# Optimization experiments

Hardware: AMD Instinct MI355X
Metric: run time of the kernel (lower is better)

## Reference

```python
import jax, jax.numpy as jnp
import numpy as np

N = 50000   # num_nodes
E = 640000  # num_edges (avg degree ~12.8)
D = 128     # input_dim
H = 128     # hidden_dim
T = 100     # targets per head


def setup_inputs() -> dict:
    key = jax.random.key(0)
    ks = jax.random.split(key, 20)
    w = lambda k, s: jax.random.normal(k, s, jnp.float32) * 0.02
    return {
        "x": jax.random.normal(ks[0], (N, D), jnp.float32),
        "edge_index": jax.random.randint(ks[1], (2, E), 0, N, dtype=jnp.int32),
        "edge_weight": jax.random.uniform(ks[2], (E,), jnp.float32),
        "ace_idx": jax.random.randint(ks[3], (T,), 0, N, dtype=jnp.int32),
        "h2_idx": jax.random.randint(ks[4], (T,), 0, N, dtype=jnp.int32),
        "W1": w(ks[5], (D, H)), "b1": jnp.zeros((H,), jnp.float32),
        "W2": w(ks[6], (H, H)), "b2": jnp.zeros((H,), jnp.float32),
        "W3": w(ks[7], (H, H)), "b3": jnp.zeros((H,), jnp.float32),
        "Wh": w(ks[8], (H, H)), "bh": jnp.zeros((H,), jnp.float32),
        "Wace": w(ks[9], (H, 1)), "bace": jnp.zeros((1,), jnp.float32),
        "Wh2": w(ks[10], (H, 1)), "bh2": jnp.zeros((1,), jnp.float32),
    }


def gcn_conv(x, src, dst, ew, W, b):
    # PyG GCNConv: add self-loops (weight 1), symmetric D^-1/2 (A+I) D^-1/2, then XW + b
    n = x.shape[0]
    xw = x @ W                                             # [N, H]
    deg = jax.ops.segment_sum(ew, dst, num_segments=n) + 1.0  # +1 from self-loop
    dinv = jax.lax.rsqrt(jnp.maximum(deg, 1e-12))          # deg >= 1 here
    norm = dinv[src] * ew * dinv[dst]                      # per-edge coefficient
    agg = jax.ops.segment_sum(norm[:, None] * xw[src], dst, num_segments=n)
    agg = agg + (dinv * dinv)[:, None] * xw                # self-loop contribution
    return agg + b


def reference(x, edge_index, edge_weight, ace_idx, h2_idx,
              W1, b1, W2, b2, W3, b3, Wh, bh, Wace, bace, Wh2, bh2):
    src, dst = edge_index[0], edge_index[1]
    h = jax.nn.relu(gcn_conv(x, src, dst, edge_weight, W1, b1))
    h = jax.nn.relu(gcn_conv(h, src, dst, edge_weight, W2, b2))
    h = jax.nn.relu(gcn_conv(h, src, dst, edge_weight, W3, b3))
    # dropout is identity in eval mode
    h = jax.nn.relu(h @ Wh + bh)
    ace_pred = h[ace_idx] @ Wace + bace   # [T, 1]
    h2_pred = h[h2_idx] @ Wh2 + bh2       # [T, 1]
    return jnp.concatenate([ace_pred, h2_pred], axis=0)  # [2T, 1]
```

## Files before the change

### kernel.cpp

```cpp
#include <hip/hip_runtime.h>
#include <math.h>

constexpr int N = 50000;
constexpr int E = 640000;
constexpr int D = 128;
constexpr int T = 100;
constexpr int MAXDEG = 64;
constexpr float SC = 256.0f;
constexpr float SCINV = 1.0f / 256.0f;
constexpr int GB = (N + 127) / 128;
constexpr int ESL = E / 4;
constexpr int EB4 = ESL / 256;
constexpr int ZB = N * 8 / 16 / 256 + 1;
constexpr int WCB = 3 * 16384 / 256;

typedef __attribute__((ext_vector_type(8))) _Float16 half8v;
typedef __attribute__((ext_vector_type(8))) unsigned short ushort8v;
typedef __attribute__((ext_vector_type(4))) float f32x4;

__device__ inline float dinv_of(unsigned int degY) {
  return 1.0f / sqrtf((float)degY * (1.0f / 16777216.0f) + 1.0f);
}


__global__ __launch_bounds__(256) void init_kernel(
    const float* __restrict__ W1, const float* __restrict__ W2,
    const float* __restrict__ W3, uint4* __restrict__ degcnt_v,
    unsigned short* __restrict__ wt0, unsigned short* __restrict__ wt1,
    unsigned short* __restrict__ w3kn) {
  int b = blockIdx.x, tid = threadIdx.x;
  if (b < ZB) {
    int i = b * 256 + tid;
    if (i < N * 8 / 16) degcnt_v[i] = uint4{0, 0, 0, 0};
  } else {
    int idx = (b - ZB) * 256 + tid;
    int layer = idx >> 14;
    int r = idx & 16383;
    if (layer == 0) {
      int n = r >> 7, k = r & 127;
      _Float16 h = (_Float16)(W1[k * D + n] * SC);
      wt0[n * D + k] = *(unsigned short*)&h;
    } else if (layer == 1) {
      int n = r >> 7, k = r & 127;
      _Float16 h = (_Float16)W2[k * D + n];
      wt1[n * D + k] = *(unsigned short*)&h;
    } else {
      int k = r >> 7, n = r & 127;
      _Float16 h = (_Float16)W3[k * D + n];
      w3kn[k * D + n] = *(unsigned short*)&h;
    }
  }
}


__global__ __launch_bounds__(256) void fused_eg1_kernel(
    const float* __restrict__ ew, const int* __restrict__ src,
    const int* __restrict__ dst,
    unsigned long long* __restrict__ degcnt, unsigned int* __restrict__ slot,
    const float* __restrict__ x, const unsigned short* __restrict__ Bt,
    unsigned short* __restrict__ z1) {
  const int b = blockIdx.x;
  const int tid = threadIdx.x;
  if (b < EB4) {
    int gid = b * 256 + tid;
    float w0 = ew[gid + 0 * ESL], w1 = ew[gid + 1 * ESL];
    float w2 = ew[gid + 2 * ESL], w3 = ew[gid + 3 * ESL];
    int d0 = dst[gid + 0 * ESL], d1 = dst[gid + 1 * ESL];
    int d2 = dst[gid + 2 * ESL], d3 = dst[gid + 3 * ESL];
    int s0 = src[gid + 0 * ESL], s1 = src[gid + 1 * ESL];
    int s2 = src[gid + 2 * ESL], s3 = src[gid + 3 * ESL];
#pragma unroll
    for (int j = 0; j < 4; ++j) {
      float w = j == 0 ? w0 : j == 1 ? w1 : j == 2 ? w2 : w3;
      int d   = j == 0 ? d0 : j == 1 ? d1 : j == 2 ? d2 : d3;
      int s   = j == 0 ? s0 : j == 1 ? s1 : j == 2 ? s2 : s3;
      unsigned int fxdeg = __float2uint_rn(w * 16777216.0f);
      unsigned int fx16 = __float2uint_rn(w * 65536.0f);
      if (fx16 > 65535u) fx16 = 65535u;
      unsigned long long old = atomicAdd(&degcnt[d],
                                         ((unsigned long long)fxdeg << 32) | 1ull);
      unsigned int rank = (unsigned int)(old & 0xffffffffull);
      if (rank < MAXDEG)
        slot[(size_t)d * MAXDEG + rank] = (fx16 << 16) | (unsigned int)s;
    }
  } else {
    const int w = tid >> 6, lane = tid & 63;
    const int q = lane >> 4, n16 = lane & 15;
    const int rbase = w * 32;
    const int row0 = (b - EB4) * 128;
    size_t arow[2];
#pragma unroll
    for (int rt = 0; rt < 2; ++rt) {
      int gr = row0 + rbase + rt * 16 + n16;
      if (gr >= N) gr = N - 1;
      arow[rt] = (size_t)gr * D;
    }
    half8v a[4][2];
#pragma unroll
    for (int kc = 0; kc < 4; ++kc) {
      const int ko = kc * 32 + q * 8;
#pragma unroll
      for (int rt = 0; rt < 2; ++rt) {
        float4 v0 = *(const float4*)&x[arow[rt] + ko];
        float4 v1 = *(const float4*)&x[arow[rt] + ko + 4];
        half8v h;
        h[0] = (_Float16)v0.x; h[1] = (_Float16)v0.y;
        h[2] = (_Float16)v0.z; h[3] = (_Float16)v0.w;
        h[4] = (_Float16)v1.x; h[5] = (_Float16)v1.y;
        h[6] = (_Float16)v1.z; h[7] = (_Float16)v1.w;
        a[kc][rt] = h;
      }
    }
    f32x4 acc[2][8] = {};
#pragma unroll
    for (int kc = 0; kc < 4; ++kc) {
      const int ko = kc * 32 + q * 8;
#pragma unroll
      for (int ct = 0; ct < 8; ++ct) {
        int n = ct * 16 + n16;
        half8v bb = *(const half8v*)&Bt[n * D + ko];
#pragma unroll
        for (int rt = 0; rt < 2; ++rt) {
          acc[rt][ct] = __builtin_amdgcn_mfma_f32_16x16x32_f16(a[kc][rt], bb, acc[rt][ct], 0, 0, 0);
        }
      }
    }
#pragma unroll
    for (int rt = 0; rt < 2; ++rt) {
#pragma unroll
      for (int r = 0; r < 4; ++r) {
        int gr = row0 + rbase + rt * 16 + q * 4 + r;
        if (gr < N) {
#pragma unroll
          for (int ct = 0; ct < 8; ++ct) {
            int col = ct * 16 + n16;
            _Float16 h = (_Float16)acc[rt][ct][r];
            z1[(size_t)gr * D + col] = *(unsigned short*)&h;
          }
        }
      }
    }
  }
}


__global__ __launch_bounds__(256) void gemm2_kernel(
    const unsigned short* __restrict__ A, const unsigned short* __restrict__ Bt,
    const uint2* __restrict__ degcnt, unsigned short* __restrict__ out) {
  const int tid = threadIdx.x;
  const int w = tid >> 6, lane = tid & 63;
  const int q = lane >> 4, n16 = lane & 15;
  const int rbase = w * 32;
  const int row0 = blockIdx.x * 128;

  size_t arow[2];
#pragma unroll
  for (int rt = 0; rt < 2; ++rt) {
    int gr = row0 + rbase + rt * 16 + n16;
    if (gr >= N) gr = N - 1;
    arow[rt] = (size_t)gr * D;
  }
  half8v a[4][2];
#pragma unroll
  for (int kc = 0; kc < 4; ++kc) {
    const int ko = kc * 32 + q * 8;
#pragma unroll
    for (int rt = 0; rt < 2; ++rt)
      a[kc][rt] = *(const half8v*)&A[arow[rt] + ko];
  }
  f32x4 acc[2][8] = {};
#pragma unroll
  for (int kc = 0; kc < 4; ++kc) {
    const int ko = kc * 32 + q * 8;
#pragma unroll
    for (int ct = 0; ct < 8; ++ct) {
      int n = ct * 16 + n16;
      half8v b = *(const half8v*)&Bt[n * D + ko];
#pragma unroll
      for (int rt = 0; rt < 2; ++rt) {
        acc[rt][ct] = __builtin_amdgcn_mfma_f32_16x16x32_f16(a[kc][rt], b, acc[rt][ct], 0, 0, 0);
      }
    }
  }
#pragma unroll
  for (int rt = 0; rt < 2; ++rt) {
#pragma unroll
    for (int r = 0; r < 4; ++r) {
      int gr = row0 + rbase + rt * 16 + q * 4 + r;
      if (gr < N) {
        float dv = dinv_of(degcnt[gr].y);
#pragma unroll
        for (int ct = 0; ct < 8; ++ct) {
          int col = ct * 16 + n16;
          _Float16 h = (_Float16)(acc[rt][ct][r] * dv);
          out[(size_t)gr * D + col] = *(unsigned short*)&h;
        }
      }
    }
  }
}


__global__ __launch_bounds__(256) void agg_kernel(
    const unsigned short* __restrict__ z, const unsigned int* __restrict__ slot,
    const uint2* __restrict__ degcnt, const float* __restrict__ bias,
    unsigned short* __restrict__ oP) {
  int g = (blockIdx.x * 256 + threadIdx.x) >> 4;
  int lane = threadIdx.x & 15;
  const unsigned int* degY = (const unsigned int*)degcnt;

  uint2 pg = degcnt[g];
  int cnt = (int)pg.x; if (cnt > MAXDEG) cnt = MAXDEG;
  float dvg = dinv_of(pg.y);
  half8v xv = *(const half8v*)&z[(size_t)g * D + lane * 8];
  float acc[8];
#pragma unroll
  for (int i = 0; i < 8; ++i) acc[i] = dvg * (float)xv[i];

  const unsigned int* sl = slot + (size_t)g * MAXDEG;
  int k = 0;
  for (; k + 4 <= cnt; k += 4) {
    uint4 p = *(const uint4*)&sl[k];
    float d0 = dinv_of(degY[((p.x & 0xffffu) << 1) + 1]);
    float d1 = dinv_of(degY[((p.y & 0xffffu) << 1) + 1]);
    float d2 = dinv_of(degY[((p.z & 0xffffu) << 1) + 1]);
    float d3 = dinv_of(degY[((p.w & 0xffffu) << 1) + 1]);
    float c0 = (float)(p.x >> 16) * (1.0f / 65536.0f) * d0;
    float c1 = (float)(p.y >> 16) * (1.0f / 65536.0f) * d1;
    float c2 = (float)(p.z >> 16) * (1.0f / 65536.0f) * d2;
    float c3 = (float)(p.w >> 16) * (1.0f / 65536.0f) * d3;
    half8v v0 = *(const half8v*)&z[(size_t)(p.x & 0xffffu) * D + lane * 8];
    half8v v1 = *(const half8v*)&z[(size_t)(p.y & 0xffffu) * D + lane * 8];
    half8v v2 = *(const half8v*)&z[(size_t)(p.z & 0xffffu) * D + lane * 8];
    half8v v3 = *(const half8v*)&z[(size_t)(p.w & 0xffffu) * D + lane * 8];
#pragma unroll
    for (int i = 0; i < 8; ++i) {
      acc[i] = fmaf(c0, (float)v0[i], acc[i]);
      acc[i] = fmaf(c1, (float)v1[i], acc[i]);
      acc[i] = fmaf(c2, (float)v2[i], acc[i]);
      acc[i] = fmaf(c3, (float)v3[i], acc[i]);
    }
  }
  for (; k < cnt; ++k) {
    unsigned int p = sl[k];
    float dsv = dinv_of(degY[((p & 0xffffu) << 1) + 1]);
    float c = (float)(p >> 16) * (1.0f / 65536.0f) * dsv;
    half8v v = *(const half8v*)&z[(size_t)(p & 0xffffu) * D + lane * 8];
#pragma unroll
    for (int i = 0; i < 8; ++i) acc[i] = fmaf(c, (float)v[i], acc[i]);
  }

  half8v hv;
#pragma unroll
  for (int i = 0; i < 8; ++i)
    hv[i] = (_Float16)fmaxf(fmaf(dvg, acc[i], bias[lane * 8 + i] * SC), 0.f);
  *(half8v*)&oP[(size_t)g * D + lane * 8] = hv;
}


__global__ __launch_bounds__(256) void l23_part_kernel(
    const unsigned short* __restrict__ z2, const unsigned int* __restrict__ slot,
    const uint2* __restrict__ degcnt, const float* __restrict__ b2,
    const int* __restrict__ ace_idx, const int* __restrict__ h2_idx,
    float* __restrict__ pacc) {
  __shared__ float sacc[16][128];
  int b = blockIdx.x;
  int t = b >> 2, p = b & 3;
  int tid = threadIdx.x;
  int node = (t < T) ? ace_idx[t] : h2_idx[t - T];

  int grp = tid >> 4, lane = tid & 15;
  int G = p * 16 + grp;
  float b2l[8];
#pragma unroll
  for (int i = 0; i < 8; ++i) b2l[i] = b2[lane * 8 + i] * SC;

  uint2 pn = degcnt[node];
  int tcnt = (int)pn.x; if (tcnt > MAXDEG) tcnt = MAXDEG;
  const unsigned int* tsl = slot + (size_t)node * MAXDEG;
  int nitems = 1 + tcnt;
  float a[8] = {};
  for (int it = G; it < nitems; it += 64) {
    int u; float wgt;
    if (it == 0) { u = node; wgt = 1.0f; }
    else {
      unsigned int pk = tsl[it - 1];
      wgt = (float)(pk >> 16) * (1.0f / 65536.0f);
      u = (int)(pk & 0xffffu);
    }
    uint2 pu = degcnt[u];
    float dvu = dinv_of(pu.y);
    int cu = (int)pu.x; if (cu > MAXDEG) cu = MAXDEG;
    half8v xv = *(const half8v*)&z2[(size_t)u * D + lane * 8];
    float r[8];
#pragma unroll
    for (int i = 0; i < 8; ++i) r[i] = (float)xv[i];
    const unsigned int* usl = slot + (size_t)u * MAXDEG;
    int e = 0;
    for (; e + 4 <= cu; e += 4) {
      uint4 p4 = *(const uint4*)&usl[e];
      float c0 = (float)(p4.x >> 16) * (1.0f / 65536.0f);
      float c1 = (float)(p4.y >> 16) * (1.0f / 65536.0f);
      float c2 = (float)(p4.z >> 16) * (1.0f / 65536.0f);
      float c3 = (float)(p4.w >> 16) * (1.0f / 65536.0f);
      half8v v0 = *(const half8v*)&z2[(size_t)(p4.x & 0xffffu) * D + lane * 8];
      half8v v1 = *(const half8v*)&z2[(size_t)(p4.y & 0xffffu) * D + lane * 8];
      half8v v2 = *(const half8v*)&z2[(size_t)(p4.z & 0xffffu) * D + lane * 8];
      half8v v3 = *(const half8v*)&z2[(size_t)(p4.w & 0xffffu) * D + lane * 8];
#pragma unroll
      for (int i = 0; i < 8; ++i) {
        r[i] = fmaf(c0, (float)v0[i], r[i]);
        r[i] = fmaf(c1, (float)v1[i], r[i]);
        r[i] = fmaf(c2, (float)v2[i], r[i]);
        r[i] = fmaf(c3, (float)v3[i], r[i]);
      }
    }
    for (; e < cu; ++e) {
      unsigned int p2 = usl[e];
      float c2 = (float)(p2 >> 16) * (1.0f / 65536.0f);
      half8v v = *(const half8v*)&z2[(size_t)(p2 & 0xffffu) * D + lane * 8];
#pragma unroll
      for (int i = 0; i < 8; ++i) r[i] = fmaf(c2, (float)v[i], r[i]);
    }
#pragma unroll
    for (int i = 0; i < 8; ++i) {
      float h2 = fmaxf(fmaf(dvu, r[i], b2l[i]), 0.f);
      a[i] = fmaf(wgt, dvu * h2, a[i]);
    }
  }
#pragma unroll
  for (int i = 0; i < 8; ++i) sacc[grp][lane * 8 + i] = a[i];
  __syncthreads();

  if (tid < 128) {
    float s = 0.f;
#pragma unroll
    for (int gp = 0; gp < 16; ++gp) s += sacc[gp][tid];
    pacc[(size_t)(t * 4 + p) * 128 + tid] = s;
  }
}


__global__ __launch_bounds__(256) void l23_finish_kernel(
    const uint2* __restrict__ degcnt, const float* __restrict__ pacc,
    const float* __restrict__ b3, const unsigned short* __restrict__ w3kn,
    const float* __restrict__ Wh, const float* __restrict__ bh,
    const int* __restrict__ ace_idx, const int* __restrict__ h2_idx,
    const float* __restrict__ Wace, const float* __restrict__ bace,
    const float* __restrict__ Wh2, const float* __restrict__ bh2,
    float* __restrict__ out) {
  __shared__ unsigned short w3l[16384];
  __shared__ float svec[128];
  __shared__ float h3v[128];
  __shared__ float psum[2];
  int t = blockIdx.x;
  int tid = threadIdx.x;
  int node; const float* whead; float bhead;
  if (t < T) { node = ace_idx[t];     whead = Wace; bhead = bace[0]; }
  else       { node = h2_idx[t - T];  whead = Wh2;  bhead = bh2[0]; }

#pragma unroll
  for (int it = 0; it < 8; ++it) {
    int idx = tid + it * 256;
    *(ushort8v*)&w3l[idx * 8] = *(const ushort8v*)&w3kn[idx * 8];
  }
  if (tid < 128) {
    const float* pa = &pacc[(size_t)t * 4 * 128];
    float s = pa[tid] + pa[128 + tid] + pa[256 + tid] + pa[384 + tid];
    svec[tid] = s * dinv_of(degcnt[node].y);
  }
  __syncthreads();

  if (tid < 128) {
    float y = b3[tid] * SC;
#pragma unroll 16
    for (int k = 0; k < 128; ++k) {
      _Float16 wv = *(const _Float16*)&w3l[k * D + tid];
      y = fmaf(svec[k], (float)wv, y);
    }
    h3v[tid] = fmaxf(y, 0.f) * SCINV;
  }
  __syncthreads();

  float v = 0.f;
  if (tid < 128) {
    float acc = bh[tid];
#pragma unroll 16
    for (int k = 0; k < 128; ++k)
      acc = fmaf(h3v[k], Wh[k * D + tid], acc);
    v = fmaxf(acc, 0.f) * whead[tid];
  }
#pragma unroll
  for (int off = 32; off; off >>= 1) v += __shfl_down(v, off, 64);
  if (tid < 128 && (tid & 63) == 0) psum[tid >> 6] = v;
  __syncthreads();
  if (tid == 0) out[t] = psum[0] + psum[1] + bhead;
}


extern "C" void kernel_launch(void* const* d_in, const int* in_sizes, int n_in,
                              void* d_out, int out_size, void* d_ws, size_t ws_size,
                              hipStream_t stream) {
  const float* x    = (const float*)d_in[0];
  const int*   ei   = (const int*)d_in[1];
  const float* ew   = (const float*)d_in[2];
  const int*   ace  = (const int*)d_in[3];
  const int*   h2   = (const int*)d_in[4];
  const float* W1 = (const float*)d_in[5];  const float* b1 = (const float*)d_in[6];
  const float* W2 = (const float*)d_in[7];  const float* b2 = (const float*)d_in[8];
  const float* W3 = (const float*)d_in[9];  const float* b3 = (const float*)d_in[10];
  const float* Wh = (const float*)d_in[11]; const float* bh = (const float*)d_in[12];
  const float* Wace = (const float*)d_in[13]; const float* bace = (const float*)d_in[14];
  const float* Wh2  = (const float*)d_in[15]; const float* bh2  = (const float*)d_in[16];
  const int* src = ei;
  const int* dst = ei + E;

  char* w = (char*)d_ws;
  unsigned long long* degcnt = (unsigned long long*)w;  w += (size_t)N * 8;
  unsigned int* slot = (unsigned int*)w;  w += (size_t)N * MAXDEG * 4;
  unsigned short* wt0 = (unsigned short*)w;  w += 16384 * 2;
  unsigned short* wt1 = (unsigned short*)w;  w += 16384 * 2;
  unsigned short* w3kn = (unsigned short*)w; w += 16384 * 2;
  float* pacc = (float*)w;                   w += (size_t)2 * T * 4 * 128 * 4;
  unsigned short* zbuf = (unsigned short*)w; w += (size_t)N * D * 2;
  unsigned short* P1  = (unsigned short*)w;  w += (size_t)N * D * 2;

  const int AG = N * 16 / 256;

  init_kernel<<<ZB + WCB, 256, 0, stream>>>(W1, W2, W3, (uint4*)degcnt, wt0, wt1, w3kn);
  fused_eg1_kernel<<<EB4 + GB, 256, 0, stream>>>(ew, src, dst, degcnt, slot, x, wt0, zbuf);
  agg_kernel<<<AG, 256, 0, stream>>>(zbuf, slot, (const uint2*)degcnt, b1, P1);
  gemm2_kernel<<<GB, 256, 0, stream>>>(P1, wt1, (const uint2*)degcnt, zbuf);
  l23_part_kernel<<<4 * 2 * T, 256, 0, stream>>>(zbuf, slot, (const uint2*)degcnt,
                                                 b2, ace, h2, pacc);
  l23_finish_kernel<<<2 * T, 256, 0, stream>>>((const uint2*)degcnt, pacc, b3, w3kn,
                                               Wh, bh, ace, h2,
                                               Wace, bace, Wh2, bh2, (float*)d_out);
}
```

Baseline: 212.4 us.

## Pad per-node degree counters to 64 bytes and split edge pass from GEMM1

Each node's 64-bit degree/count atomic now sits at a stride of eight words (64 bytes), so concurrent atomics to neighbouring nodes no longer share a cache line. The fused edge/GEMM1 kernel is split into a simple one-edge-per-thread edge pass and a separate GEMM1 kernel. The cost is an 8x larger degree array to zero and scattered, poorly cached degree reads in the aggregation kernels. Splitting the kernels also gives up the overlap between atomics and MFMA work within a single launch.

```diff
diff --git a/kernel.cpp b/kernel.cpp
--- a/kernel.cpp
+++ b/kernel.cpp
@@ -6,12 +6,12 @@
 constexpr int D = 128;
 constexpr int T = 100;
 constexpr int MAXDEG = 64;
+constexpr int PAD = 8;
 constexpr float SC = 256.0f;
 constexpr float SCINV = 1.0f / 256.0f;
 constexpr int GB = (N + 127) / 128;
-constexpr int ESL = E / 4;
-constexpr int EB4 = ESL / 256;
-constexpr int ZB = N * 8 / 16 / 256 + 1;
+constexpr int EBLK = (E + 255) / 256;
+constexpr int ZB = (N * 4 + 255) / 256;
 constexpr int WCB = 3 * 16384 / 256;
 
 typedef __attribute__((ext_vector_type(8))) _Float16 half8v;
@@ -31,7 +31,7 @@
   int b = blockIdx.x, tid = threadIdx.x;
   if (b < ZB) {
     int i = b * 256 + tid;
-    if (i < N * 8 / 16) degcnt_v[i] = uint4{0, 0, 0, 0};
+    if (i < N * 4) degcnt_v[i] = uint4{0, 0, 0, 0};
   } else {
     int idx = (b - ZB) * 256 + tid;
     int layer = idx >> 14;
@@ -53,106 +53,34 @@
 }
 
 
-__global__ __launch_bounds__(256) void fused_eg1_kernel(
-    const float* __restrict__ ew, const int* __restrict__ src,
-    const int* __restrict__ dst,
-    unsigned long long* __restrict__ degcnt, unsigned int* __restrict__ slot,
+__global__ void edge_pass_kernel(const float* __restrict__ ew, const int* __restrict__ src,
+                                 const int* __restrict__ dst,
+                                 unsigned long long* __restrict__ degcnt,
+                                 unsigned int* __restrict__ slot) {
+  int e = blockIdx.x * 256 + threadIdx.x;
+  if (e < E) {
+    float w = ew[e];
+    int d = dst[e];
+    unsigned int fxdeg = __float2uint_rn(w * 16777216.0f);
+    unsigned int fx16 = __float2uint_rn(w * 65536.0f);
+    if (fx16 > 65535u) fx16 = 65535u;
+    unsigned long long old = atomicAdd(&degcnt[(size_t)d * PAD],
+                                       ((unsigned long long)fxdeg << 32) | 1ull);
+    unsigned int rank = (unsigned int)(old & 0xffffffffull);
+    if (rank < MAXDEG)
+      slot[(size_t)d * MAXDEG + rank] = (fx16 << 16) | (unsigned int)src[e];
+  }
+}
+
+
+__global__ __launch_bounds__(256) void gemm1_kernel(
     const float* __restrict__ x, const unsigned short* __restrict__ Bt,
     unsigned short* __restrict__ z1) {
-  const int b = blockIdx.x;
-  const int tid = threadIdx.x;
-  if (b < EB4) {
-    int gid = b * 256 + tid;
-    float w0 = ew[gid + 0 * ESL], w1 = ew[gid + 1 * ESL];
-    float w2 = ew[gid + 2 * ESL], w3 = ew[gid + 3 * ESL];
-    int d0 = dst[gid + 0 * ESL], d1 = dst[gid + 1 * ESL];
-    int d2 = dst[gid + 2 * ESL], d3 = dst[gid + 3 * ESL];
-    int s0 = src[gid + 0 * ESL], s1 = src[gid + 1 * ESL];
-    int s2 = src[gid + 2 * ESL], s3 = src[gid + 3 * ESL];
-#pragma unroll
-    for (int j = 0; j < 4; ++j) {
-      float w = j == 0 ? w0 : j == 1 ? w1 : j == 2 ? w2 : w3;
-      int d   = j == 0 ? d0 : j == 1 ? d1 : j == 2 ? d2 : d3;
-      int s   = j == 0 ? s0 : j == 1 ? s1 : j == 2 ? s2 : s3;
-      unsigned int fxdeg = __float2uint_rn(w * 16777216.0f);
-      unsigned int fx16 = __float2uint_rn(w * 65536.0f);
-      if (fx16 > 65535u) fx16 = 65535u;
-      unsigned long long old = atomicAdd(&degcnt[d],
-                                         ((unsigned long long)fxdeg << 32) | 1ull);
-      unsigned int rank = (unsigned int)(old & 0xffffffffull);
-      if (rank < MAXDEG)
-        slot[(size_t)d * MAXDEG + rank] = (fx16 << 16) | (unsigned int)s;
-    }
-  } else {
-    const int w = tid >> 6, lane = tid & 63;
-    const int q = lane >> 4, n16 = lane & 15;
-    const int rbase = w * 32;
-    const int row0 = (b - EB4) * 128;
-    size_t arow[2];
-#pragma unroll
-    for (int rt = 0; rt < 2; ++rt) {
-      int gr = row0 + rbase + rt * 16 + n16;
-      if (gr >= N) gr = N - 1;
-      arow[rt] = (size_t)gr * D;
-    }
-    half8v a[4][2];
-#pragma unroll
-    for (int kc = 0; kc < 4; ++kc) {
-      const int ko = kc * 32 + q * 8;
-#pragma unroll
-      for (int rt = 0; rt < 2; ++rt) {
-        float4 v0 = *(const float4*)&x[arow[rt] + ko];
-        float4 v1 = *(const float4*)&x[arow[rt] + ko + 4];
-        half8v h;
-        h[0] = (_Float16)v0.x; h[1] = (_Float16)v0.y;
-        h[2] = (_Float16)v0.z; h[3] = (_Float16)v0.w;
-        h[4] = (_Float16)v1.x; h[5] = (_Float16)v1.y;
-        h[6] = (_Float16)v1.z; h[7] = (_Float16)v1.w;
-        a[kc][rt] = h;
-      }
-    }
-    f32x4 acc[2][8] = {};
-#pragma unroll
-    for (int kc = 0; kc < 4; ++kc) {
-      const int ko = kc * 32 + q * 8;
-#pragma unroll
-      for (int ct = 0; ct < 8; ++ct) {
-        int n = ct * 16 + n16;
-        half8v bb = *(const half8v*)&Bt[n * D + ko];
-#pragma unroll
-        for (int rt = 0; rt < 2; ++rt) {
-          acc[rt][ct] = __builtin_amdgcn_mfma_f32_16x16x32_f16(a[kc][rt], bb, acc[rt][ct], 0, 0, 0);
-        }
-      }
-    }
-#pragma unroll
-    for (int rt = 0; rt < 2; ++rt) {
-#pragma unroll
-      for (int r = 0; r < 4; ++r) {
-        int gr = row0 + rbase + rt * 16 + q * 4 + r;
-        if (gr < N) {
-#pragma unroll
-          for (int ct = 0; ct < 8; ++ct) {
-            int col = ct * 16 + n16;
-            _Float16 h = (_Float16)acc[rt][ct][r];
-            z1[(size_t)gr * D + col] = *(unsigned short*)&h;
-          }
-        }
-      }
-    }
-  }
-}
-
-
-__global__ __launch_bounds__(256) void gemm2_kernel(
-    const unsigned short* __restrict__ A, const unsigned short* __restrict__ Bt,
-    const uint2* __restrict__ degcnt, unsigned short* __restrict__ out) {
   const int tid = threadIdx.x;
   const int w = tid >> 6, lane = tid & 63;
   const int q = lane >> 4, n16 = lane & 15;
   const int rbase = w * 32;
   const int row0 = blockIdx.x * 128;
-
   size_t arow[2];
 #pragma unroll
   for (int rt = 0; rt < 2; ++rt) {
@@ -165,6 +93,70 @@
   for (int kc = 0; kc < 4; ++kc) {
     const int ko = kc * 32 + q * 8;
 #pragma unroll
+    for (int rt = 0; rt < 2; ++rt) {
+      float4 v0 = *(const float4*)&x[arow[rt] + ko];
+      float4 v1 = *(const float4*)&x[arow[rt] + ko + 4];
+      half8v h;
+      h[0] = (_Float16)v0.x; h[1] = (_Float16)v0.y;
+      h[2] = (_Float16)v0.z; h[3] = (_Float16)v0.w;
+      h[4] = (_Float16)v1.x; h[5] = (_Float16)v1.y;
+      h[6] = (_Float16)v1.z; h[7] = (_Float16)v1.w;
+      a[kc][rt] = h;
+    }
+  }
+  f32x4 acc[2][8] = {};
+#pragma unroll
+  for (int kc = 0; kc < 4; ++kc) {
+    const int ko = kc * 32 + q * 8;
+#pragma unroll
+    for (int ct = 0; ct < 8; ++ct) {
+      int n = ct * 16 + n16;
+      half8v bb = *(const half8v*)&Bt[n * D + ko];
+#pragma unroll
+      for (int rt = 0; rt < 2; ++rt) {
+        acc[rt][ct] = __builtin_amdgcn_mfma_f32_16x16x32_f16(a[kc][rt], bb, acc[rt][ct], 0, 0, 0);
+      }
+    }
+  }
+#pragma unroll
+  for (int rt = 0; rt < 2; ++rt) {
+#pragma unroll
+    for (int r = 0; r < 4; ++r) {
+      int gr = row0 + rbase + rt * 16 + q * 4 + r;
+      if (gr < N) {
+#pragma unroll
+        for (int ct = 0; ct < 8; ++ct) {
+          int col = ct * 16 + n16;
+          _Float16 h = (_Float16)acc[rt][ct][r];
+          z1[(size_t)gr * D + col] = *(unsigned short*)&h;
+        }
+      }
+    }
+  }
+}
+
+
+__global__ __launch_bounds__(256) void gemm2_kernel(
+    const unsigned short* __restrict__ A, const unsigned short* __restrict__ Bt,
+    const uint2* __restrict__ degcnt2, unsigned short* __restrict__ out) {
+  const int tid = threadIdx.x;
+  const int w = tid >> 6, lane = tid & 63;
+  const int q = lane >> 4, n16 = lane & 15;
+  const int rbase = w * 32;
+  const int row0 = blockIdx.x * 128;
+
+  size_t arow[2];
+#pragma unroll
+  for (int rt = 0; rt < 2; ++rt) {
+    int gr = row0 + rbase + rt * 16 + n16;
+    if (gr >= N) gr = N - 1;
+    arow[rt] = (size_t)gr * D;
+  }
+  half8v a[4][2];
+#pragma unroll
+  for (int kc = 0; kc < 4; ++kc) {
+    const int ko = kc * 32 + q * 8;
+#pragma unroll
     for (int rt = 0; rt < 2; ++rt)
       a[kc][rt] = *(const half8v*)&A[arow[rt] + ko];
   }
@@ -188,7 +180,7 @@
     for (int r = 0; r < 4; ++r) {
       int gr = row0 + rbase + rt * 16 + q * 4 + r;
       if (gr < N) {
-        float dv = dinv_of(degcnt[gr].y);
+        float dv = dinv_of(degcnt2[(size_t)gr * PAD].y);
 #pragma unroll
         for (int ct = 0; ct < 8; ++ct) {
           int col = ct * 16 + n16;
@@ -203,13 +195,13 @@
 
 __global__ __launch_bounds__(256) void agg_kernel(
     const unsigned short* __restrict__ z, const unsigned int* __restrict__ slot,
-    const uint2* __restrict__ degcnt, const float* __restrict__ bias,
+    const uint2* __restrict__ degcnt2, const float* __restrict__ bias,
     unsigned short* __restrict__ oP) {
   int g = (blockIdx.x * 256 + threadIdx.x) >> 4;
   int lane = threadIdx.x & 15;
-  const unsigned int* degY = (const unsigned int*)degcnt;
-
-  uint2 pg = degcnt[g];
+  const unsigned int* degY = (const unsigned int*)degcnt2;
+
+  uint2 pg = degcnt2[(size_t)g * PAD];
   int cnt = (int)pg.x; if (cnt > MAXDEG) cnt = MAXDEG;
   float dvg = dinv_of(pg.y);
   half8v xv = *(const half8v*)&z[(size_t)g * D + lane * 8];
@@ -221,10 +213,10 @@
   int k = 0;
   for (; k + 4 <= cnt; k += 4) {
     uint4 p = *(const uint4*)&sl[k];
-    float d0 = dinv_of(degY[((p.x & 0xffffu) << 1) + 1]);
-    float d1 = dinv_of(degY[((p.y & 0xffffu) << 1) + 1]);
-    float d2 = dinv_of(degY[((p.z & 0xffffu) << 1) + 1]);
-    float d3 = dinv_of(degY[((p.w & 0xffffu) << 1) + 1]);
+    float d0 = dinv_of(degY[((size_t)(p.x & 0xffffu) * 2 * PAD) + 1]);
+    float d1 = dinv_of(degY[((size_t)(p.y & 0xffffu) * 2 * PAD) + 1]);
+    float d2 = dinv_of(degY[((size_t)(p.z & 0xffffu) * 2 * PAD) + 1]);
+    float d3 = dinv_of(degY[((size_t)(p.w & 0xffffu) * 2 * PAD) + 1]);
     float c0 = (float)(p.x >> 16) * (1.0f / 65536.0f) * d0;
     float c1 = (float)(p.y >> 16) * (1.0f / 65536.0f) * d1;
     float c2 = (float)(p.z >> 16) * (1.0f / 65536.0f) * d2;
@@ -243,7 +235,7 @@
   }
   for (; k < cnt; ++k) {
     unsigned int p = sl[k];
-    float dsv = dinv_of(degY[((p & 0xffffu) << 1) + 1]);
+    float dsv = dinv_of(degY[((size_t)(p & 0xffffu) * 2 * PAD) + 1]);
     float c = (float)(p >> 16) * (1.0f / 65536.0f) * dsv;
     half8v v = *(const half8v*)&z[(size_t)(p & 0xffffu) * D + lane * 8];
 #pragma unroll
@@ -260,7 +252,7 @@
 
 __global__ __launch_bounds__(256) void l23_part_kernel(
     const unsigned short* __restrict__ z2, const unsigned int* __restrict__ slot,
-    const uint2* __restrict__ degcnt, const float* __restrict__ b2,
+    const uint2* __restrict__ degcnt2, const float* __restrict__ b2,
     const int* __restrict__ ace_idx, const int* __restrict__ h2_idx,
     float* __restrict__ pacc) {
   __shared__ float sacc[16][128];
@@ -275,7 +267,7 @@
 #pragma unroll
   for (int i = 0; i < 8; ++i) b2l[i] = b2[lane * 8 + i] * SC;
 
-  uint2 pn = degcnt[node];
+  uint2 pn = degcnt2[(size_t)node * PAD];
   int tcnt = (int)pn.x; if (tcnt > MAXDEG) tcnt = MAXDEG;
   const unsigned int* tsl = slot + (size_t)node * MAXDEG;
   int nitems = 1 + tcnt;
@@ -288,7 +280,7 @@
       wgt = (float)(pk >> 16) * (1.0f / 65536.0f);
       u = (int)(pk & 0xffffu);
     }
-    uint2 pu = degcnt[u];
+    uint2 pu = degcnt2[(size_t)u * PAD];
     float dvu = dinv_of(pu.y);
     int cu = (int)pu.x; if (cu > MAXDEG) cu = MAXDEG;
     half8v xv = *(const half8v*)&z2[(size_t)u * D + lane * 8];
@@ -342,7 +334,7 @@
 
 
 __global__ __launch_bounds__(256) void l23_finish_kernel(
-    const uint2* __restrict__ degcnt, const float* __restrict__ pacc,
+    const uint2* __restrict__ degcnt2, const float* __restrict__ pacc,
     const float* __restrict__ b3, const unsigned short* __restrict__ w3kn,
     const float* __restrict__ Wh, const float* __restrict__ bh,
     const int* __restrict__ ace_idx, const int* __restrict__ h2_idx,
@@ -367,7 +359,7 @@
   if (tid < 128) {
     const float* pa = &pacc[(size_t)t * 4 * 128];
     float s = pa[tid] + pa[128 + tid] + pa[256 + tid] + pa[384 + tid];
-    svec[tid] = s * dinv_of(degcnt[node].y);
+    svec[tid] = s * dinv_of(degcnt2[(size_t)node * PAD].y);
   }
   __syncthreads();
 
@@ -416,7 +408,7 @@
   const int* dst = ei + E;
 
   char* w = (char*)d_ws;
-  unsigned long long* degcnt = (unsigned long long*)w;  w += (size_t)N * 8;
+  unsigned long long* degcnt = (unsigned long long*)w;  w += (size_t)N * PAD * 8;
   unsigned int* slot = (unsigned int*)w;  w += (size_t)N * MAXDEG * 4;
   unsigned short* wt0 = (unsigned short*)w;  w += 16384 * 2;
   unsigned short* wt1 = (unsigned short*)w;  w += 16384 * 2;
@@ -428,7 +420,8 @@
   const int AG = N * 16 / 256;
 
   init_kernel<<<ZB + WCB, 256, 0, stream>>>(W1, W2, W3, (uint4*)degcnt, wt0, wt1, w3kn);
-  fused_eg1_kernel<<<EB4 + GB, 256, 0, stream>>>(ew, src, dst, degcnt, slot, x, wt0, zbuf);
+  edge_pass_kernel<<<EBLK, 256, 0, stream>>>(ew, src, dst, degcnt, slot);
+  gemm1_kernel<<<GB, 256, 0, stream>>>(x, wt0, zbuf);
   agg_kernel<<<AG, 256, 0, stream>>>(zbuf, slot, (const uint2*)degcnt, b1, P1);
   gemm2_kernel<<<GB, 256, 0, stream>>>(P1, wt1, (const uint2*)degcnt, zbuf);
   l23_part_kernel<<<4 * 2 * T, 256, 0, stream>>>(zbuf, slot, (const uint2*)degcnt,
```

Result: slower. 219.8 us (+3.5%).

## Fuse layer-3 finish into partial kernel via last-block counter; reorder GEMM/edge blocks

Applied to the files above, without the earlier changes.

Merges the l23 partial and finish kernels into one launch. Each of the four partial blocks per target bumps an atomic counter, and the last one to arrive does the W3/head computation, which removes a kernel launch and its dependency gap. The fused layer-1 kernel now places the GEMM blocks first and switches the edge-bucketing part to one edge per thread instead of four strided edges. The counter array is zeroed in init_kernel, and the change adds shared memory pressure plus atomic ordering that must be correct.

```diff
diff --git a/kernel.cpp b/kernel.cpp
--- a/kernel.cpp
+++ b/kernel.cpp
@@ -9,9 +9,9 @@
 constexpr float SC = 256.0f;
 constexpr float SCINV = 1.0f / 256.0f;
 constexpr int GB = (N + 127) / 128;
-constexpr int ESL = E / 4;
-constexpr int EB4 = ESL / 256;
-constexpr int ZB = N * 8 / 16 / 256 + 1;
+constexpr int EBLK = (E + 255) / 256;
+constexpr int ZTOT = (N * 8 + 2048) / 16;
+constexpr int ZB = (ZTOT + 255) / 256;
 constexpr int WCB = 3 * 16384 / 256;
 
 typedef __attribute__((ext_vector_type(8))) _Float16 half8v;
@@ -25,13 +25,13 @@
 
 __global__ __launch_bounds__(256) void init_kernel(
     const float* __restrict__ W1, const float* __restrict__ W2,
-    const float* __restrict__ W3, uint4* __restrict__ degcnt_v,
+    const float* __restrict__ W3, uint4* __restrict__ zero_v,
     unsigned short* __restrict__ wt0, unsigned short* __restrict__ wt1,
     unsigned short* __restrict__ w3kn) {
   int b = blockIdx.x, tid = threadIdx.x;
   if (b < ZB) {
     int i = b * 256 + tid;
-    if (i < N * 8 / 16) degcnt_v[i] = uint4{0, 0, 0, 0};
+    if (i < ZTOT) zero_v[i] = uint4{0, 0, 0, 0};
   } else {
     int idx = (b - ZB) * 256 + tid;
     int layer = idx >> 14;
@@ -53,27 +53,19 @@
 }
 
 
-__global__ __launch_bounds__(256) void fused_eg1_kernel(
+__global__ __launch_bounds__(256) void fused_g1e_kernel(
+    const float* __restrict__ x, const unsigned short* __restrict__ Bt,
+    unsigned short* __restrict__ z1,
     const float* __restrict__ ew, const int* __restrict__ src,
     const int* __restrict__ dst,
-    unsigned long long* __restrict__ degcnt, unsigned int* __restrict__ slot,
-    const float* __restrict__ x, const unsigned short* __restrict__ Bt,
-    unsigned short* __restrict__ z1) {
+    unsigned long long* __restrict__ degcnt, unsigned int* __restrict__ slot) {
   const int b = blockIdx.x;
   const int tid = threadIdx.x;
-  if (b < EB4) {
-    int gid = b * 256 + tid;
-    float w0 = ew[gid + 0 * ESL], w1 = ew[gid + 1 * ESL];
-    float w2 = ew[gid + 2 * ESL], w3 = ew[gid + 3 * ESL];
-    int d0 = dst[gid + 0 * ESL], d1 = dst[gid + 1 * ESL];
-    int d2 = dst[gid + 2 * ESL], d3 = dst[gid + 3 * ESL];
-    int s0 = src[gid + 0 * ESL], s1 = src[gid + 1 * ESL];
-    int s2 = src[gid + 2 * ESL], s3 = src[gid + 3 * ESL];
-#pragma unroll
-    for (int j = 0; j < 4; ++j) {
-      float w = j == 0 ? w0 : j == 1 ? w1 : j == 2 ? w2 : w3;
-      int d   = j == 0 ? d0 : j == 1 ? d1 : j == 2 ? d2 : d3;
-      int s   = j == 0 ? s0 : j == 1 ? s1 : j == 2 ? s2 : s3;
+  if (b >= GB) {
+    int e = (b - GB) * 256 + tid;
+    if (e < E) {
+      float w = ew[e];
+      int d = dst[e];
       unsigned int fxdeg = __float2uint_rn(w * 16777216.0f);
       unsigned int fx16 = __float2uint_rn(w * 65536.0f);
       if (fx16 > 65535u) fx16 = 65535u;
@@ -81,62 +73,62 @@
                                          ((unsigned long long)fxdeg << 32) | 1ull);
       unsigned int rank = (unsigned int)(old & 0xffffffffull);
       if (rank < MAXDEG)
-        slot[(size_t)d * MAXDEG + rank] = (fx16 << 16) | (unsigned int)s;
-    }
-  } else {
-    const int w = tid >> 6, lane = tid & 63;
-    const int q = lane >> 4, n16 = lane & 15;
-    const int rbase = w * 32;
-    const int row0 = (b - EB4) * 128;
-    size_t arow[2];
+        slot[(size_t)d * MAXDEG + rank] = (fx16 << 16) | (unsigned int)src[e];
+    }
+    return;
+  }
+  const int w = tid >> 6, lane = tid & 63;
+  const int q = lane >> 4, n16 = lane & 15;
+  const int rbase = w * 32;
+  const int row0 = b * 128;
+  size_t arow[2];
+#pragma unroll
+  for (int rt = 0; rt < 2; ++rt) {
+    int gr = row0 + rbase + rt * 16 + n16;
+    if (gr >= N) gr = N - 1;
+    arow[rt] = (size_t)gr * D;
+  }
+  half8v a[4][2];
+#pragma unroll
+  for (int kc = 0; kc < 4; ++kc) {
+    const int ko = kc * 32 + q * 8;
 #pragma unroll
     for (int rt = 0; rt < 2; ++rt) {
-      int gr = row0 + rbase + rt * 16 + n16;
-      if (gr >= N) gr = N - 1;
-      arow[rt] = (size_t)gr * D;
-    }
-    half8v a[4][2];
-#pragma unroll
-    for (int kc = 0; kc < 4; ++kc) {
-      const int ko = kc * 32 + q * 8;
+      float4 v0 = *(const float4*)&x[arow[rt] + ko];
+      float4 v1 = *(const float4*)&x[arow[rt] + ko + 4];
+      half8v h;
+      h[0] = (_Float16)v0.x; h[1] = (_Float16)v0.y;
+      h[2] = (_Float16)v0.z; h[3] = (_Float16)v0.w;
+      h[4] = (_Float16)v1.x; h[5] = (_Float16)v1.y;
+      h[6] = (_Float16)v1.z; h[7] = (_Float16)v1.w;
+      a[kc][rt] = h;
+    }
+  }
+  f32x4 acc[2][8] = {};
+#pragma unroll
+  for (int kc = 0; kc < 4; ++kc) {
+    const int ko = kc * 32 + q * 8;
+#pragma unroll
+    for (int ct = 0; ct < 8; ++ct) {
+      int n = ct * 16 + n16;
+      half8v bb = *(const half8v*)&Bt[n * D + ko];
 #pragma unroll
       for (int rt = 0; rt < 2; ++rt) {
-        float4 v0 = *(const float4*)&x[arow[rt] + ko];
-        float4 v1 = *(const float4*)&x[arow[rt] + ko + 4];
-        half8v h;
-        h[0] = (_Float16)v0.x; h[1] = (_Float16)v0.y;
-        h[2] = (_Float16)v0.z; h[3] = (_Float16)v0.w;
-        h[4] = (_Float16)v1.x; h[5] = (_Float16)v1.y;
-        h[6] = (_Float16)v1.z; h[7] = (_Float16)v1.w;
-        a[kc][rt] = h;
+        acc[rt][ct] = __builtin_amdgcn_mfma_f32_16x16x32_f16(a[kc][rt], bb, acc[rt][ct], 0, 0, 0);
       }
     }
-    f32x4 acc[2][8] = {};
-#pragma unroll
-    for (int kc = 0; kc < 4; ++kc) {
-      const int ko = kc * 32 + q * 8;
-#pragma unroll
-      for (int ct = 0; ct < 8; ++ct) {
-        int n = ct * 16 + n16;
-        half8v bb = *(const half8v*)&Bt[n * D + ko];
-#pragma unroll
-        for (int rt = 0; rt < 2; ++rt) {
-          acc[rt][ct] = __builtin_amdgcn_mfma_f32_16x16x32_f16(a[kc][rt], bb, acc[rt][ct], 0, 0, 0);
-        }
-      }
-    }
-#pragma unroll
-    for (int rt = 0; rt < 2; ++rt) {
-#pragma unroll
-      for (int r = 0; r < 4; ++r) {
-        int gr = row0 + rbase + rt * 16 + q * 4 + r;
-        if (gr < N) {
-#pragma unroll
-          for (int ct = 0; ct < 8; ++ct) {
-            int col = ct * 16 + n16;
-            _Float16 h = (_Float16)acc[rt][ct][r];
-            z1[(size_t)gr * D + col] = *(unsigned short*)&h;
-          }
+  }
+#pragma unroll
+  for (int rt = 0; rt < 2; ++rt) {
+#pragma unroll
+    for (int r = 0; r < 4; ++r) {
+      int gr = row0 + rbase + rt * 16 + q * 4 + r;
+      if (gr < N) {
+#pragma unroll
+        for (int ct = 0; ct < 8; ++ct) {
+          int col = ct * 16 + n16;
+          _Float16 h = (_Float16)acc[rt][ct][r];
+          z1[(size_t)gr * D + col] = *(unsigned short*)&h;
         }
       }
     }
@@ -258,12 +250,22 @@
 }
 
 
-__global__ __launch_bounds__(256) void l23_part_kernel(
+__global__ __launch_bounds__(256) void l23_pf_kernel(
     const unsigned short* __restrict__ z2, const unsigned int* __restrict__ slot,
     const uint2* __restrict__ degcnt, const float* __restrict__ b2,
+    const float* __restrict__ b3, const unsigned short* __restrict__ w3kn,
+    const float* __restrict__ Wh, const float* __restrict__ bh,
     const int* __restrict__ ace_idx, const int* __restrict__ h2_idx,
-    float* __restrict__ pacc) {
+    const float* __restrict__ Wace, const float* __restrict__ bace,
+    const float* __restrict__ Wh2, const float* __restrict__ bh2,
+    float* __restrict__ pacc, unsigned int* __restrict__ done,
+    float* __restrict__ out) {
   __shared__ float sacc[16][128];
+  __shared__ unsigned short w3l[16384];
+  __shared__ float svec[128];
+  __shared__ float h3v[128];
+  __shared__ float psum[2];
+  __shared__ int amLast;
   int b = blockIdx.x;
   int t = b >> 2, p = b & 3;
   int tid = threadIdx.x;
@@ -336,38 +338,33 @@
     float s = 0.f;
 #pragma unroll
     for (int gp = 0; gp < 16; ++gp) s += sacc[gp][tid];
-    pacc[(size_t)(t * 4 + p) * 128 + tid] = s;
-  }
-}
-
-
-__global__ __launch_bounds__(256) void l23_finish_kernel(
-    const uint2* __restrict__ degcnt, const float* __restrict__ pacc,
-    const float* __restrict__ b3, const unsigned short* __restrict__ w3kn,
-    const float* __restrict__ Wh, const float* __restrict__ bh,
-    const int* __restrict__ ace_idx, const int* __restrict__ h2_idx,
-    const float* __restrict__ Wace, const float* __restrict__ bace,
-    const float* __restrict__ Wh2, const float* __restrict__ bh2,
-    float* __restrict__ out) {
-  __shared__ unsigned short w3l[16384];
-  __shared__ float svec[128];
-  __shared__ float h3v[128];
-  __shared__ float psum[2];
-  int t = blockIdx.x;
-  int tid = threadIdx.x;
-  int node; const float* whead; float bhead;
-  if (t < T) { node = ace_idx[t];     whead = Wace; bhead = bace[0]; }
-  else       { node = h2_idx[t - T];  whead = Wh2;  bhead = bh2[0]; }
-
+    __hip_atomic_store(&pacc[(size_t)(t * 4 + p) * 128 + tid], s,
+                       __ATOMIC_RELAXED, __HIP_MEMORY_SCOPE_AGENT);
+  }
+  __syncthreads();
+  if (tid == 0) {
+    unsigned int old = __hip_atomic_fetch_add(&done[t], 1u,
+                                              __ATOMIC_ACQ_REL, __HIP_MEMORY_SCOPE_AGENT);
+    amLast = (old == 3u);
+  }
+  __syncthreads();
+  if (!amLast) return;
+
+  const float* whead; float bhead;
+  if (t < T) { whead = Wace; bhead = bace[0]; }
+  else       { whead = Wh2;  bhead = bh2[0]; }
 #pragma unroll
   for (int it = 0; it < 8; ++it) {
     int idx = tid + it * 256;
     *(ushort8v*)&w3l[idx * 8] = *(const ushort8v*)&w3kn[idx * 8];
   }
   if (tid < 128) {
-    const float* pa = &pacc[(size_t)t * 4 * 128];
-    float s = pa[tid] + pa[128 + tid] + pa[256 + tid] + pa[384 + tid];
-    svec[tid] = s * dinv_of(degcnt[node].y);
+    float s = 0.f;
+#pragma unroll
+    for (int qq = 0; qq < 4; ++qq)
+      s += __hip_atomic_load(&pacc[(size_t)(t * 4 + qq) * 128 + tid],
+                             __ATOMIC_RELAXED, __HIP_MEMORY_SCOPE_AGENT);
+    svec[tid] = s * dinv_of(pn.y);
   }
   __syncthreads();
 
@@ -417,7 +414,8 @@
 
   char* w = (char*)d_ws;
   unsigned long long* degcnt = (unsigned long long*)w;  w += (size_t)N * 8;
-  unsigned int* slot = (unsigned int*)w;  w += (size_t)N * MAXDEG * 4;
+  unsigned int* done = (unsigned int*)w;     w += 2048;
+  unsigned int* slot = (unsigned int*)w;     w += (size_t)N * MAXDEG * 4;
   unsigned short* wt0 = (unsigned short*)w;  w += 16384 * 2;
   unsigned short* wt1 = (unsigned short*)w;  w += 16384 * 2;
   unsigned short* w3kn = (unsigned short*)w; w += 16384 * 2;
@@ -428,12 +426,11 @@
   const int AG = N * 16 / 256;
 
   init_kernel<<<ZB + WCB, 256, 0, stream>>>(W1, W2, W3, (uint4*)degcnt, wt0, wt1, w3kn);
-  fused_eg1_kernel<<<EB4 + GB, 256, 0, stream>>>(ew, src, dst, degcnt, slot, x, wt0, zbuf);
+  fused_g1e_kernel<<<GB + EBLK, 256, 0, stream>>>(x, wt0, zbuf, ew, src, dst, degcnt, slot);
   agg_kernel<<<AG, 256, 0, stream>>>(zbuf, slot, (const uint2*)degcnt, b1, P1);
   gemm2_kernel<<<GB, 256, 0, stream>>>(P1, wt1, (const uint2*)degcnt, zbuf);
-  l23_part_kernel<<<4 * 2 * T, 256, 0, stream>>>(zbuf, slot, (const uint2*)degcnt,
-                                                 b2, ace, h2, pacc);
-  l23_finish_kernel<<<2 * T, 256, 0, stream>>>((const uint2*)degcnt, pacc, b3, w3kn,
-                                               Wh, bh, ace, h2,
-                                               Wace, bace, Wh2, bh2, (float*)d_out);
-}
+  l23_pf_kernel<<<4 * 2 * T, 256, 0, stream>>>(zbuf, slot, (const uint2*)degcnt,
+                                               b2, b3, w3kn, Wh, bh, ace, h2,
+                                               Wace, bace, Wh2, bh2,
+                                               pacc, done, (float*)d_out);
+}
```

After: 225.3 us. +6.1%, slower.
